# Kernel optimization log

Measured on AMD Instinct MI355X. Metric: run time of the kernel, lower is better.

Reference implementation:

```python
import jax, jax.numpy as jnp
import numpy as np

EMB = 128
SQRT_EMB = 128 ** 0.5
LOGIT_CLIP = 10.0


def setup_inputs() -> dict:
    key = jax.random.key(0)
    ks = jax.random.split(key, 10)
    B, N, M, D = 128, 512, 512, EMB
    s = 1.0 / np.sqrt(D)
    return {
        "encoded_last_node": jax.random.normal(ks[0], (B, N, D), jnp.float32),
        "load": jax.random.uniform(ks[1], (B, N), jnp.float32),
        "cur_dist": jax.random.uniform(ks[2], (B, N, M), jnp.float32),
        "log_scale": jnp.ones((), jnp.float32),
        "ninf_mask": jnp.zeros((B, N, M), jnp.float32),
        "encoded_nodes": jax.random.normal(ks[3], (B, M, D), jnp.float32),
        "Wq_last": jax.random.normal(ks[4], (D, D + 1), jnp.float32) * s,
        "Wk": jax.random.normal(ks[5], (D, D), jnp.float32) * s,
        "Wv": jax.random.normal(ks[6], (D, D), jnp.float32) * s,
        "alpha1": jnp.ones((1,), jnp.float32),
        "alpha2": jnp.ones((1,), jnp.float32),
    }


def reference(encoded_last_node, load, cur_dist, log_scale, ninf_mask,
              encoded_nodes, Wq_last, Wk, Wv, alpha1, alpha2):
    # set_kv
    k = jnp.einsum('bmd,ed->bme', encoded_nodes, Wk)   # (B,M,D)
    v = jnp.einsum('bmd,ed->bme', encoded_nodes, Wv)   # (B,M,D)
    # query from last node + load
    input_cat = jnp.concatenate([encoded_last_node, load[:, :, None]], axis=2)  # (B,N,D+1)
    q = jnp.einsum('bnc,ec->bne', input_cat, Wq_last)  # (B,N,D)
    # AAFM: exp-bias linear attention with sigmoid gate
    adaptation_bias = -alpha1[0] * log_scale * cur_dist + ninf_mask  # (B,N,M)
    eb = jnp.exp(adaptation_bias)
    ek = jnp.exp(k)
    num = jnp.einsum('bnm,bmd->bnd', eb, ek * v)
    den = jnp.einsum('bnm,bmd->bnd', eb, ek)
    weighted = jnp.nan_to_num(num / den)  # mirrors torch nan_to_num correction
    aafm_out = jax.nn.sigmoid(q) * weighted  # (B,N,D)
    # single-head decode score against encoder embeddings
    score = jnp.einsum('bnd,bmd->bnm', aafm_out, encoded_nodes)
    score_scaled = score / SQRT_EMB - alpha2[0] * log_scale * cur_dist
    score_masked = LOGIT_CLIP * jnp.tanh(score_scaled) + ninf_mask
    probs = jax.nn.softmax(score_masked, axis=-1)
    return probs
```

## Files before the change

kernel.cpp:

```cpp
#include <hip/hip_runtime.h>
#include <math.h>

#define B 128
#define N 512
#define M 512
#define D 128

typedef __attribute__((ext_vector_type(8))) short s16x8;
typedef __attribute__((ext_vector_type(4))) short s16x4;
typedef __attribute__((ext_vector_type(4))) float f32x4;

#define MFMA16(a, b, c) __builtin_amdgcn_mfma_f32_16x16x32_bf16(a, b, c, 0, 0, 0)

#define VMCNT4()  asm volatile("s_waitcnt vmcnt(4)" ::: "memory")
#define VMCNT8()  asm volatile("s_waitcnt vmcnt(8)" ::: "memory")
#define VMCNT12() asm volatile("s_waitcnt vmcnt(12)" ::: "memory")

__device__ __forceinline__ void gload16(const void* g, void* l) {
    __builtin_amdgcn_global_load_lds(
        (const __attribute__((address_space(1))) unsigned int*)g,
        (__attribute__((address_space(3))) unsigned int*)l, 16, 0, 0);
}

__device__ __forceinline__ float fast_tanh(float x) {
    x = fminf(fmaxf(x, -15.f), 15.f);
    float E = __expf(2.f * x);
    return 1.f - 2.f / (E + 1.f);
}

__device__ __forceinline__ unsigned short bf16rne(float x) {
    unsigned u = __float_as_uint(x);
    return (unsigned short)((u + 0x7FFF + ((u >> 16) & 1)) >> 16);
}

__device__ __forceinline__ void fsplit(float x, short& h, short& l) {
    unsigned u = __float_as_uint(x);
    h = (short)(u >> 16);
    float fh = __uint_as_float(u & 0xffff0000u);
    l = (short)(__float_as_uint(x - fh) >> 16);
}

__device__ __forceinline__ void fsplit8(float4 x0, float4 x1, s16x8& h, s16x8& l) {
    short a, b;
    fsplit(x0.x, a, b); h[0] = a; l[0] = b;
    fsplit(x0.y, a, b); h[1] = a; l[1] = b;
    fsplit(x0.z, a, b); h[2] = a; l[2] = b;
    fsplit(x0.w, a, b); h[3] = a; l[3] = b;
    fsplit(x1.x, a, b); h[4] = a; l[4] = b;
    fsplit(x1.y, a, b); h[5] = a; l[5] = b;
    fsplit(x1.z, a, b); h[6] = a; l[6] = b;
    fsplit(x1.w, a, b); h[7] = a; l[7] = b;
}

__device__ __forceinline__ void ebsplit(float4 c0, float4 c1, float4 f0, float4 f1,
                                        float a1ls, s16x8& ah, s16x8& al) {
    float4 e0, e1;
    e0.x = __expf(fmaf(-a1ls, c0.x, f0.x));
    e0.y = __expf(fmaf(-a1ls, c0.y, f0.y));
    e0.z = __expf(fmaf(-a1ls, c0.z, f0.z));
    e0.w = __expf(fmaf(-a1ls, c0.w, f0.w));
    e1.x = __expf(fmaf(-a1ls, c1.x, f1.x));
    e1.y = __expf(fmaf(-a1ls, c1.y, f1.y));
    e1.z = __expf(fmaf(-a1ls, c1.z, f1.z));
    e1.w = __expf(fmaf(-a1ls, c1.w, f1.w));
    fsplit8(e0, e1, ah, al);
}

__global__ void k_prep_w(const float* __restrict__ Wk, const float* __restrict__ Wv,
                         const float* __restrict__ Wq,
                         unsigned short* __restrict__ Wk_hi, unsigned short* __restrict__ Wk_lo,
                         unsigned short* __restrict__ Wv_hi, unsigned short* __restrict__ Wv_lo,
                         unsigned short* __restrict__ Wq_hi, unsigned short* __restrict__ Wq_lo) {
    int i = blockIdx.x * 256 + threadIdx.x;
    short h, l;
    if (i < 16384) {
        fsplit(Wk[i], h, l); Wk_hi[i] = (unsigned short)h; Wk_lo[i] = (unsigned short)l;
    } else if (i < 32768) {
        int j = i - 16384;
        fsplit(Wv[j], h, l); Wv_hi[j] = (unsigned short)h; Wv_lo[j] = (unsigned short)l;
    } else {
        int j = i - 32768; int e = j >> 7, d = j & 127;
        fsplit(Wq[e * 129 + d], h, l); Wq_hi[j] = (unsigned short)h; Wq_lo[j] = (unsigned short)l;
    }
}

__global__ __launch_bounds__(256) void k_kv(const float* __restrict__ enc,
        const unsigned short* __restrict__ Wk_hi, const unsigned short* __restrict__ Wk_lo,
        const unsigned short* __restrict__ Wv_hi, const unsigned short* __restrict__ Wv_lo,
        unsigned short* __restrict__ EKb, unsigned short* __restrict__ EKVb) {
    int b = blockIdx.y;
    int wave = threadIdx.x >> 6, lane = threadIdx.x & 63;
    int row = lane & 15, kg = lane >> 4;
    int m0 = blockIdx.x * 64 + wave * 16;
    f32x4 acc[16];
#pragma unroll
    for (int i = 0; i < 16; i++) acc[i] = (f32x4)0.f;
    const float* ap = enc + ((size_t)b * M + m0 + row) * D + kg * 8;
#pragma unroll
    for (int ks = 0; ks < 4; ks++) {
        float4 x0 = *(const float4*)(ap + ks * 32);
        float4 x1 = *(const float4*)(ap + ks * 32 + 4);
        s16x8 ah, al;
        fsplit8(x0, x1, ah, al);
        int wb = ks * 32 + kg * 8;
#pragma unroll
        for (int ct = 0; ct < 8; ct++) {
            int e = ct * 16 + row;
            s16x8 bh = *(const s16x8*)(Wk_hi + e * D + wb);
            s16x8 bl = *(const s16x8*)(Wk_lo + e * D + wb);
            acc[ct] = MFMA16(ah, bh, acc[ct]);
            acc[ct] = MFMA16(al, bh, acc[ct]);
            acc[ct] = MFMA16(ah, bl, acc[ct]);
            bh = *(const s16x8*)(Wv_hi + e * D + wb);
            bl = *(const s16x8*)(Wv_lo + e * D + wb);
            acc[8 + ct] = MFMA16(ah, bh, acc[8 + ct]);
            acc[8 + ct] = MFMA16(al, bh, acc[8 + ct]);
            acc[8 + ct] = MFMA16(ah, bl, acc[8 + ct]);
        }
    }
#pragma unroll
    for (int ct = 0; ct < 8; ct++) {
        int e = ct * 16 + row;
        s16x4 kb, vb;
#pragma unroll
        for (int r = 0; r < 4; r++) {
            float ek = __expf(acc[ct][r]);
            float ev = ek * acc[8 + ct][r];
            kb[r] = (short)bf16rne(ek);
            vb[r] = (short)bf16rne(ev);
        }
        int m = m0 + kg * 4;
        int chunk = (m & 31) >> 3;
        int p = chunk ^ (e & 3);
        size_t o = ((size_t)b * D + e) * M + (size_t)(m & ~31) + p * 8 + (m & 7);
        *(s16x4*)(EKb + o) = kb;
        *(s16x4*)(EKVb + o) = vb;
    }
}

__global__ __launch_bounds__(256) void k_q(const float* __restrict__ encl,
        const float* __restrict__ loadv, const float* __restrict__ Wq,
        const unsigned short* __restrict__ Wq_hi, const unsigned short* __restrict__ Wq_lo,
        float* __restrict__ SQ) {
    int b = blockIdx.y;
    int wave = threadIdx.x >> 6, lane = threadIdx.x & 63;
    int row = lane & 15, kg = lane >> 4;
    int n0 = blockIdx.x * 64 + wave * 16;
    f32x4 acc[8];
#pragma unroll
    for (int i = 0; i < 8; i++) acc[i] = (f32x4)0.f;
    const float* ap = encl + ((size_t)b * N + n0 + row) * D + kg * 8;
#pragma unroll
    for (int ks = 0; ks < 4; ks++) {
        float4 x0 = *(const float4*)(ap + ks * 32);
        float4 x1 = *(const float4*)(ap + ks * 32 + 4);
        s16x8 ah, al;
        fsplit8(x0, x1, ah, al);
        int wb = ks * 32 + kg * 8;
#pragma unroll
        for (int ct = 0; ct < 8; ct++) {
            int e = ct * 16 + row;
            s16x8 bh = *(const s16x8*)(Wq_hi + e * D + wb);
            s16x8 bl = *(const s16x8*)(Wq_lo + e * D + wb);
            acc[ct] = MFMA16(ah, bh, acc[ct]);
            acc[ct] = MFMA16(al, bh, acc[ct]);
            acc[ct] = MFMA16(ah, bl, acc[ct]);
        }
    }
#pragma unroll
    for (int r = 0; r < 4; r++) {
        int n = n0 + kg * 4 + r;
        float lv = loadv[(size_t)b * N + n];
        size_t ro = ((size_t)b * N + n) * D;
#pragma unroll
        for (int ct = 0; ct < 8; ct++) {
            int e = ct * 16 + row;
            float q = acc[ct][r] + lv * Wq[e * 129 + 128];
            SQ[ro + e] = 1.f / (1.f + __expf(-q));
        }
    }
}

__global__ __launch_bounds__(256, 3) void k_numden(
        const float* __restrict__ cd, const float* __restrict__ ninf,
        const unsigned short* __restrict__ EKVb, const unsigned short* __restrict__ EKb,
        float* __restrict__ SQ,
        const float* __restrict__ a1p, const float* __restrict__ lsp) {
    int o = blockIdx.x;
    int xcd = o & 7, j = o >> 3;
    int b = ((j >> 3) << 3) + xcd;
    int nb = j & 7;
    int w = threadIdx.x >> 6, lane = threadIdx.x & 63;
    int ns = w >> 1, eh = w & 1;
    int row = lane & 15, kg = lane >> 4;
    int n0 = nb * 64 + ns * 32;
    __shared__ __align__(16) char lds[3][16384];
    float a1ls = a1p[0] * lsp[0];
    const char* gEKV = (const char*)EKVb + (size_t)b * D * M * 2;
    const char* gEK  = (const char*)EKb  + (size_t)b * D * M * 2;
    f32x4 accN[2][4], accD[2][4];
#pragma unroll
    for (int s = 0; s < 2; s++)
#pragma unroll
        for (int i = 0; i < 4; i++) { accN[s][i] = (f32x4)0.f; accD[s][i] = (f32x4)0.f; }
    const float* cdp0 = cd + ((size_t)b * N + n0 + row) * M + kg * 8;
    const float* nfp0 = ninf + ((size_t)b * N + n0 + row) * M + kg * 8;
    const float* cdp1 = cdp0 + (size_t)16 * M;
    const float* nfp1 = nfp0 + (size_t)16 * M;
    int rbase = eh * 4096 + row * 64 + ((kg ^ (row & 3)) << 4);

#define STAGE_ND(ldsbase, mt)                                                    \
    _Pragma("unroll")                                                            \
    for (int jv = 0; jv < 4; jv++) {                                             \
        int idx = jv * 256 + threadIdx.x;                                        \
        const char* gb = (idx >> 9) ? gEK : gEKV;                                \
        int rem = idx & 511;                                                     \
        gload16(gb + (size_t)(rem >> 2) * 1024 + (size_t)(mt) * 64 + (rem & 3) * 16, \
                (char*)(ldsbase) + idx * 16);                                    \
    }

    float4 c00 = *(const float4*)(cdp0), c01 = *(const float4*)(cdp0 + 4);
    float4 f00 = *(const float4*)(nfp0), f01 = *(const float4*)(nfp0 + 4);
    float4 c10 = *(const float4*)(cdp1), c11 = *(const float4*)(cdp1 + 4);
    float4 f10 = *(const float4*)(nfp1), f11 = *(const float4*)(nfp1 + 4);
    STAGE_ND((char*)lds, 0)
    STAGE_ND((char*)lds + 16384, 1)

#pragma unroll
    for (int mt = 0; mt < 16; mt++) {
        if (mt == 0) { VMCNT4(); } else if (mt == 15) { VMCNT8(); } else { VMCNT12(); }
        __builtin_amdgcn_s_barrier();
        __builtin_amdgcn_sched_barrier(0);
        float4 nc00, nc01, nf00, nf01, nc10, nc11, nf10, nf11;
        if (mt < 15) {
            int m = (mt + 1) * 32;
            nc00 = *(const float4*)(cdp0 + m); nc01 = *(const float4*)(cdp0 + m + 4);
            nf00 = *(const float4*)(nfp0 + m); nf01 = *(const float4*)(nfp0 + m + 4);
            nc10 = *(const float4*)(cdp1 + m); nc11 = *(const float4*)(cdp1 + m + 4);
            nf10 = *(const float4*)(nfp1 + m); nf11 = *(const float4*)(nfp1 + m + 4);
        }
        if (mt < 14) STAGE_ND((char*)lds + ((mt + 2) % 3) * 16384, mt + 2)
        s16x8 ah0, al0, ah1, al1;
        ebsplit(c00, c01, f00, f01, a1ls, ah0, al0);
        ebsplit(c10, c11, f10, f11, a1ls, ah1, al1);
        const char* L = (const char*)lds + (mt % 3) * 16384;
#pragma unroll
        for (int ct = 0; ct < 4; ct++) {
            int ro = ct * 1024 + rbase;
            s16x8 bv = *(const s16x8*)(L + ro);
            s16x8 bk = *(const s16x8*)(L + 8192 + ro);
            accN[0][ct] = MFMA16(ah0, bv, accN[0][ct]);
            accN[0][ct] = MFMA16(al0, bv, accN[0][ct]);
            accN[1][ct] = MFMA16(ah1, bv, accN[1][ct]);
            accN[1][ct] = MFMA16(al1, bv, accN[1][ct]);
            accD[0][ct] = MFMA16(ah0, bk, accD[0][ct]);
            accD[0][ct] = MFMA16(al0, bk, accD[0][ct]);
            accD[1][ct] = MFMA16(ah1, bk, accD[1][ct]);
            accD[1][ct] = MFMA16(al1, bk, accD[1][ct]);
        }
        if (mt < 15) {
            c00 = nc00; c01 = nc01; f00 = nf00; f01 = nf01;
            c10 = nc10; c11 = nc11; f10 = nf10; f11 = nf11;
        }
    }
#pragma unroll
    for (int s = 0; s < 2; s++) {
#pragma unroll
        for (int r = 0; r < 4; r++) {
            int n = n0 + s * 16 + kg * 4 + r;
            size_t ro = ((size_t)b * N + n) * D;
#pragma unroll
            for (int ct = 0; ct < 4; ct++) {
                int e = eh * 64 + ct * 16 + row;
                float num = accN[s][ct][r], den = accD[s][ct][r];
                float ww = (den != 0.f) ? num / den : 0.f;
                float aafm = SQ[ro + e] * ww;
                unsigned u = __float_as_uint(aafm);
                unsigned hi = u >> 16;
                float fh = __uint_as_float(u & 0xffff0000u);
                unsigned lo = __float_as_uint(aafm - fh) >> 16;
                SQ[ro + e] = __uint_as_float(hi | (lo << 16));
            }
        }
    }
}

__global__ void k_encsplit(const float* __restrict__ enc,
                           unsigned short* __restrict__ Eh, unsigned short* __restrict__ El) {
    size_t i = (size_t)blockIdx.x * 256 + threadIdx.x;
    size_t bm = i >> 4;
    int c = (int)(i & 15);
    int m = (int)(bm & 511);
    int p = c ^ (m & 7);
    const float* src = enc + bm * 128 + c * 8;
    float4 x0 = *(const float4*)(src);
    float4 x1 = *(const float4*)(src + 4);
    s16x8 h, l;
    fsplit8(x0, x1, h, l);
    *(s16x8*)(Eh + bm * 128 + p * 8) = h;
    *(s16x8*)(El + bm * 128 + p * 8) = l;
}

__global__ __launch_bounds__(256, 3) void k_score(
        const float* __restrict__ AAFM,
        const unsigned short* __restrict__ Eh, const unsigned short* __restrict__ El,
        const float* __restrict__ cd, const float* __restrict__ ninf,
        const float* __restrict__ a2p, const float* __restrict__ lsp,
        float* __restrict__ out) {
    int o = blockIdx.x;
    int xcd = o & 7, j = o >> 3;
    int b = ((j >> 4) << 3) + xcd;
    int nb = j & 15;
    int n0 = nb * 32;
    int w = threadIdx.x >> 6, lane = threadIdx.x & 63;
    int row = lane & 15, kg = lane >> 4;
    int ng = w >> 1, mh = w & 1;
    __shared__ __align__(16) char lds[3][16384];
    __shared__ float redm[32][2];
    __shared__ float reds[32][2];
    float a2ls = a2p[0] * lsp[0];
    const float invs = 0.08838834764831845f;

    const float* apk = AAFM + ((size_t)b * N + n0 + ng * 16 + row) * D + kg * 8;
    s16x8 ah[4], al[4];
#pragma unroll
    for (int es = 0; es < 4; es++) {
        float4 w0 = *(const float4*)(apk + es * 32);
        float4 w1 = *(const float4*)(apk + es * 32 + 4);
        unsigned u;
        u = __float_as_uint(w0.x); ah[es][0] = (short)(u & 0xffff); al[es][0] = (short)(u >> 16);
        u = __float_as_uint(w0.y); ah[es][1] = (short)(u & 0xffff); al[es][1] = (short)(u >> 16);
        u = __float_as_uint(w0.z); ah[es][2] = (short)(u & 0xffff); al[es][2] = (short)(u >> 16);
        u = __float_as_uint(w0.w); ah[es][3] = (short)(u & 0xffff); al[es][3] = (short)(u >> 16);
        u = __float_as_uint(w1.x); ah[es][4] = (short)(u & 0xffff); al[es][4] = (short)(u >> 16);
        u = __float_as_uint(w1.y); ah[es][5] = (short)(u & 0xffff); al[es][5] = (short)(u >> 16);
        u = __float_as_uint(w1.z); ah[es][6] = (short)(u & 0xffff); al[es][6] = (short)(u >> 16);
        u = __float_as_uint(w1.w); ah[es][7] = (short)(u & 0xffff); al[es][7] = (short)(u >> 16);
    }
    f32x4 acc[16];
#pragma unroll
    for (int i = 0; i < 16; i++) acc[i] = (f32x4)0.f;

    int mloc = mh * 16 + row;
    int rbase = mloc * 256;
    int sw = mloc & 7;
    size_t rowidx[4];
#pragma unroll
    for (int r = 0; r < 4; r++)
        rowidx[r] = ((size_t)b * N + n0 + ng * 16 + kg * 4 + r) * M;

#define STAGE_SC(ldsbase, mc)                                                      \
    _Pragma("unroll")                                                              \
    for (int jv = 0; jv < 4; jv++) {                                               \
        int id = (w * 4 + jv) * 64 + lane;                                         \
        int arr = id >> 9, rem = id & 511;                                         \
        const unsigned short* gb = arr ? El : Eh;                                  \
        gload16((const char*)gb + ((size_t)b * M + (size_t)(mc) * 32) * 256 + rem * 16, \
                (char*)(ldsbase) + arr * 8192 + rem * 16);                         \
    }

    float cdv[4], nfv[4];
#pragma unroll
    for (int r = 0; r < 4; r++) {
        cdv[r] = cd[rowidx[r] + mloc];
        nfv[r] = ninf[rowidx[r] + mloc];
    }
    STAGE_SC((char*)lds, 0)
    STAGE_SC((char*)lds + 16384, 1)

#pragma unroll
    for (int mc = 0; mc < 16; mc++) {
        if (mc == 0) { VMCNT4(); } else if (mc == 15) { VMCNT8(); } else { VMCNT12(); }
        __builtin_amdgcn_s_barrier();
        __builtin_amdgcn_sched_barrier(0);
        float ncd[4], nnf[4];
        if (mc < 15) {
#pragma unroll
            for (int r = 0; r < 4; r++) {
                ncd[r] = cd[rowidx[r] + (size_t)(mc + 1) * 32 + mloc];
                nnf[r] = ninf[rowidx[r] + (size_t)(mc + 1) * 32 + mloc];
            }
        }
        if (mc < 14) STAGE_SC((char*)lds + ((mc + 2) % 3) * 16384, mc + 2)
        const char* L = (const char*)lds + (mc % 3) * 16384;
#pragma unroll
        for (int es = 0; es < 4; es++) {
            int ph = (4 * es + kg) ^ sw;
            s16x8 bh = *(const s16x8*)(L + rbase + ph * 16);
            s16x8 bl = *(const s16x8*)(L + 8192 + rbase + ph * 16);
            acc[mc] = MFMA16(ah[es], bh, acc[mc]);
            acc[mc] = MFMA16(al[es], bh, acc[mc]);
            acc[mc] = MFMA16(ah[es], bl, acc[mc]);
        }
#pragma unroll
        for (int r = 0; r < 4; r++) {
            acc[mc][r] = 10.f * fast_tanh(fmaf(acc[mc][r], invs, -a2ls * cdv[r]))
                       + nfv[r];
        }
        if (mc < 15) {
#pragma unroll
            for (int r = 0; r < 4; r++) { cdv[r] = ncd[r]; nfv[r] = nnf[r]; }
        }
    }
    float mx[4], sm[4];
#pragma unroll
    for (int r = 0; r < 4; r++) {
        float m = acc[0][r];
#pragma unroll
        for (int a = 1; a < 16; a++) m = fmaxf(m, acc[a][r]);
#pragma unroll
        for (int s = 1; s < 16; s <<= 1) m = fmaxf(m, __shfl_xor(m, s, 64));
        mx[r] = m;
    }
    int rl = ng * 16 + kg * 4;
    if (row == 0) {
#pragma unroll
        for (int r = 0; r < 4; r++) redm[rl + r][mh] = mx[r];
    }
    __syncthreads();
#pragma unroll
    for (int r = 0; r < 4; r++) {
        float m = fmaxf(redm[rl + r][0], redm[rl + r][1]);
        float s = 0.f;
#pragma unroll
        for (int a = 0; a < 16; a++) {
            float e = __expf(acc[a][r] - m);
            acc[a][r] = e;
            s += e;
        }
#pragma unroll
        for (int sh = 1; sh < 16; sh <<= 1) s += __shfl_xor(s, sh, 64);
        sm[r] = s;
    }
    if (row == 0) {
#pragma unroll
        for (int r = 0; r < 4; r++) reds[rl + r][mh] = sm[r];
    }
    __syncthreads();
#pragma unroll
    for (int r = 0; r < 4; r++) {
        float inv = 1.f / (reds[rl + r][0] + reds[rl + r][1]);
        size_t ro = ((size_t)b * N + n0 + rl + r) * M;
#pragma unroll
        for (int a = 0; a < 16; a++) {
            out[ro + a * 32 + mh * 16 + row] = acc[a][r] * inv;
        }
    }
}

extern "C" void kernel_launch(void* const* d_in, const int* in_sizes, int n_in,
                              void* d_out, int out_size, void* d_ws, size_t ws_size,
                              hipStream_t stream) {
    const float* encl  = (const float*)d_in[0];
    const float* loadv = (const float*)d_in[1];
    const float* cdist = (const float*)d_in[2];
    const float* ls    = (const float*)d_in[3];
    const float* ninf  = (const float*)d_in[4];
    const float* enc   = (const float*)d_in[5];
    const float* Wq    = (const float*)d_in[6];
    const float* Wk    = (const float*)d_in[7];
    const float* Wv    = (const float*)d_in[8];
    const float* a1    = (const float*)d_in[9];
    const float* a2    = (const float*)d_in[10];
    char* ws = (char*)d_ws;
    unsigned short* EKb     = (unsigned short*)(ws);
    unsigned short* EKVb    = (unsigned short*)(ws + 33554432);
    float*          SQ      = (float*)(ws + 67108864);
    unsigned short* Wk_hi   = (unsigned short*)(ws + 100663296);
    unsigned short* Wk_lo   = (unsigned short*)(ws + 100663296 + 32768);
    unsigned short* Wv_hi   = (unsigned short*)(ws + 100663296 + 65536);
    unsigned short* Wv_lo   = (unsigned short*)(ws + 100663296 + 98304);
    unsigned short* Wq_hi   = (unsigned short*)(ws + 100663296 + 131072);
    unsigned short* Wq_lo   = (unsigned short*)(ws + 100663296 + 163840);
    unsigned short* ENC_hi  = EKb;
    unsigned short* ENC_lo  = EKVb;
    float* out = (float*)d_out;

    k_prep_w<<<192, 256, 0, stream>>>(Wk, Wv, Wq, Wk_hi, Wk_lo, Wv_hi, Wv_lo, Wq_hi, Wq_lo);
    k_kv<<<dim3(8, 128), 256, 0, stream>>>(enc, Wk_hi, Wk_lo, Wv_hi, Wv_lo, EKb, EKVb);
    k_q<<<dim3(8, 128), 256, 0, stream>>>(encl, loadv, Wq, Wq_hi, Wq_lo, SQ);
    k_numden<<<1024, 256, 0, stream>>>(cdist, ninf, EKVb, EKb, SQ, a1, ls);
    k_encsplit<<<4096, 256, 0, stream>>>(enc, ENC_hi, ENC_lo);
    k_score<<<2048, 256, 0, stream>>>(SQ, ENC_hi, ENC_lo, cdist, ninf, a2, ls, out);
}
```

Before: 358.3 us.

## Split numden work across D instead of N and deepen A-operand prefetch

The numden kernel now assigns each block 32 query rows, with the four waves splitting the 128 output columns into 32-wide slices instead of splitting rows and halves. This doubles the grid to 2048 blocks and halves the accumulators per thread. Each wave still reads the full cur_dist/ninf tile for its rows, so those global loads are now issued four times per block instead of twice. The A-operand loads are also prefetched two iterations ahead with double-buffered registers, and the wait counts are changed to match. The goal is more parallelism and better latency hiding, at the cost of more redundant global traffic for the distance and mask inputs.

```diff
diff --git a/kernel.cpp b/kernel.cpp
--- a/kernel.cpp
+++ b/kernel.cpp
@@ -12,6 +12,7 @@
 
 #define MFMA16(a, b, c) __builtin_amdgcn_mfma_f32_16x16x32_bf16(a, b, c, 0, 0, 0)
 
+#define VMCNT0()  asm volatile("s_waitcnt vmcnt(0)" ::: "memory")
 #define VMCNT4()  asm volatile("s_waitcnt vmcnt(4)" ::: "memory")
 #define VMCNT8()  asm volatile("s_waitcnt vmcnt(8)" ::: "memory")
 #define VMCNT12() asm volatile("s_waitcnt vmcnt(12)" ::: "memory")
@@ -188,26 +189,25 @@
         const float* __restrict__ a1p, const float* __restrict__ lsp) {
     int o = blockIdx.x;
     int xcd = o & 7, j = o >> 3;
-    int b = ((j >> 3) << 3) + xcd;
-    int nb = j & 7;
+    int b = ((j >> 4) << 3) + xcd;
+    int nb = j & 15;
+    int n0 = nb * 32;
     int w = threadIdx.x >> 6, lane = threadIdx.x & 63;
-    int ns = w >> 1, eh = w & 1;
     int row = lane & 15, kg = lane >> 4;
-    int n0 = nb * 64 + ns * 32;
     __shared__ __align__(16) char lds[3][16384];
     float a1ls = a1p[0] * lsp[0];
     const char* gEKV = (const char*)EKVb + (size_t)b * D * M * 2;
     const char* gEK  = (const char*)EKb  + (size_t)b * D * M * 2;
-    f32x4 accN[2][4], accD[2][4];
+    f32x4 accN[2][2], accD[2][2];
 #pragma unroll
     for (int s = 0; s < 2; s++)
 #pragma unroll
-        for (int i = 0; i < 4; i++) { accN[s][i] = (f32x4)0.f; accD[s][i] = (f32x4)0.f; }
+        for (int i = 0; i < 2; i++) { accN[s][i] = (f32x4)0.f; accD[s][i] = (f32x4)0.f; }
     const float* cdp0 = cd + ((size_t)b * N + n0 + row) * M + kg * 8;
     const float* nfp0 = ninf + ((size_t)b * N + n0 + row) * M + kg * 8;
     const float* cdp1 = cdp0 + (size_t)16 * M;
     const float* nfp1 = nfp0 + (size_t)16 * M;
-    int rbase = eh * 4096 + row * 64 + ((kg ^ (row & 3)) << 4);
+    int rbase = w * 2048 + row * 64 + ((kg ^ (row & 3)) << 4);
 
 #define STAGE_ND(ldsbase, mt)                                                    \
     _Pragma("unroll")                                                            \
@@ -219,33 +219,38 @@
                 (char*)(ldsbase) + idx * 16);                                    \
     }
 
-    float4 c00 = *(const float4*)(cdp0), c01 = *(const float4*)(cdp0 + 4);
-    float4 f00 = *(const float4*)(nfp0), f01 = *(const float4*)(nfp0 + 4);
-    float4 c10 = *(const float4*)(cdp1), c11 = *(const float4*)(cdp1 + 4);
-    float4 f10 = *(const float4*)(nfp1), f11 = *(const float4*)(nfp1 + 4);
+    float4 Ac[2][2][2], Af[2][2][2];
+#define LOAD_A(p, mt)                                                            \
+    Ac[p][0][0] = *(const float4*)(cdp0 + (mt) * 32);                            \
+    Ac[p][0][1] = *(const float4*)(cdp0 + (mt) * 32 + 4);                        \
+    Af[p][0][0] = *(const float4*)(nfp0 + (mt) * 32);                            \
+    Af[p][0][1] = *(const float4*)(nfp0 + (mt) * 32 + 4);                        \
+    Ac[p][1][0] = *(const float4*)(cdp1 + (mt) * 32);                            \
+    Ac[p][1][1] = *(const float4*)(cdp1 + (mt) * 32 + 4);                        \
+    Af[p][1][0] = *(const float4*)(nfp1 + (mt) * 32);                            \
+    Af[p][1][1] = *(const float4*)(nfp1 + (mt) * 32 + 4);
+
+    LOAD_A(0, 0)
     STAGE_ND((char*)lds, 0)
+    LOAD_A(1, 1)
     STAGE_ND((char*)lds + 16384, 1)
 
 #pragma unroll
     for (int mt = 0; mt < 16; mt++) {
-        if (mt == 0) { VMCNT4(); } else if (mt == 15) { VMCNT8(); } else { VMCNT12(); }
+        if (mt == 15) { VMCNT0(); } else { VMCNT12(); }
         __builtin_amdgcn_s_barrier();
         __builtin_amdgcn_sched_barrier(0);
-        float4 nc00, nc01, nf00, nf01, nc10, nc11, nf10, nf11;
-        if (mt < 15) {
-            int m = (mt + 1) * 32;
-            nc00 = *(const float4*)(cdp0 + m); nc01 = *(const float4*)(cdp0 + m + 4);
-            nf00 = *(const float4*)(nfp0 + m); nf01 = *(const float4*)(nfp0 + m + 4);
-            nc10 = *(const float4*)(cdp1 + m); nc11 = *(const float4*)(cdp1 + m + 4);
-            nf10 = *(const float4*)(nfp1 + m); nf11 = *(const float4*)(nfp1 + m + 4);
-        }
-        if (mt < 14) STAGE_ND((char*)lds + ((mt + 2) % 3) * 16384, mt + 2)
+        int p = mt & 1;
         s16x8 ah0, al0, ah1, al1;
-        ebsplit(c00, c01, f00, f01, a1ls, ah0, al0);
-        ebsplit(c10, c11, f10, f11, a1ls, ah1, al1);
+        ebsplit(Ac[p][0][0], Ac[p][0][1], Af[p][0][0], Af[p][0][1], a1ls, ah0, al0);
+        ebsplit(Ac[p][1][0], Ac[p][1][1], Af[p][1][0], Af[p][1][1], a1ls, ah1, al1);
+        if (mt <= 13) {
+            LOAD_A(p, mt + 2)
+            STAGE_ND((char*)lds + ((mt + 2) % 3) * 16384, mt + 2)
+        }
         const char* L = (const char*)lds + (mt % 3) * 16384;
 #pragma unroll
-        for (int ct = 0; ct < 4; ct++) {
+        for (int ct = 0; ct < 2; ct++) {
             int ro = ct * 1024 + rbase;
             s16x8 bv = *(const s16x8*)(L + ro);
             s16x8 bk = *(const s16x8*)(L + 8192 + ro);
@@ -258,10 +263,6 @@
             accD[1][ct] = MFMA16(ah1, bk, accD[1][ct]);
             accD[1][ct] = MFMA16(al1, bk, accD[1][ct]);
         }
-        if (mt < 15) {
-            c00 = nc00; c01 = nc01; f00 = nf00; f01 = nf01;
-            c10 = nc10; c11 = nc11; f10 = nf10; f11 = nf11;
-        }
     }
 #pragma unroll
     for (int s = 0; s < 2; s++) {
@@ -270,8 +271,8 @@
             int n = n0 + s * 16 + kg * 4 + r;
             size_t ro = ((size_t)b * N + n) * D;
 #pragma unroll
-            for (int ct = 0; ct < 4; ct++) {
-                int e = eh * 64 + ct * 16 + row;
+            for (int ct = 0; ct < 2; ct++) {
+                int e = w * 32 + ct * 16 + row;
                 float num = accN[s][ct][r], den = accD[s][ct][r];
                 float ww = (den != 0.f) ? num / den : 0.f;
                 float aafm = SQ[ro + e] * ww;
@@ -479,7 +480,7 @@
     k_prep_w<<<192, 256, 0, stream>>>(Wk, Wv, Wq, Wk_hi, Wk_lo, Wv_hi, Wv_lo, Wq_hi, Wq_lo);
     k_kv<<<dim3(8, 128), 256, 0, stream>>>(enc, Wk_hi, Wk_lo, Wv_hi, Wv_lo, EKb, EKVb);
     k_q<<<dim3(8, 128), 256, 0, stream>>>(encl, loadv, Wq, Wq_hi, Wq_lo, SQ);
-    k_numden<<<1024, 256, 0, stream>>>(cdist, ninf, EKVb, EKb, SQ, a1, ls);
+    k_numden<<<2048, 256, 0, stream>>>(cdist, ninf, EKVb, EKb, SQ, a1, ls);
     k_encsplit<<<4096, 256, 0, stream>>>(enc, ENC_hi, ENC_lo);
     k_score<<<2048, 256, 0, stream>>>(SQ, ENC_hi, ENC_lo, cdist, ninf, a2, ls, out);
 }
```

Result: slower. 410.9 us (+14.7%).
